# Performance work log

Hardware: AMD Instinct MI355X
Metric: run time of the kernel (lower is better)

The kernel has to match this reference:

```python
import jax, jax.numpy as jnp
import numpy as np
from jax import lax

T = 50
THETA = 1.0 - 0.0001  # max_1 - 0.0001, max_1 = T_win/T = 1.0


def conv_t(x, w, b, pad_h):
    # x: [N, C, H, W, T]; slayer conv3d has time-kernel 1 -> conv2d per timestep.
    n, c, h, wd, t = x.shape
    xb = jnp.moveaxis(x, -1, 1).reshape(n * t, c, h, wd)
    y = lax.conv_general_dilated(xb, w, (1, 1), [(pad_h, pad_h), (0, 0)])
    y = y + b[None, :, None, None]
    o, h2, w2 = y.shape[1], y.shape[2], y.shape[3]
    return jnp.moveaxis(y.reshape(n, t, o, h2, w2), 1, -1)


def if_spikes(a):
    # catCuda.getSpikes on an input stacked T times: IF neuron with constant
    # drive a per step, soft reset (v -= theta on spike). a: [N,C,H,W].
    def step(v, _):
        v = v + a
        s = (v >= THETA).astype(a.dtype)
        return v - s * THETA, s
    _, sp = lax.scan(step, jnp.zeros_like(a), None, length=T)
    return jnp.moveaxis(sp, 0, -1)  # [N,C,H,W,T]


def setup_inputs() -> dict:
    key = jax.random.key(0)
    ks = jax.random.split(key, 6)
    def w(k, shape, scale):
        return jax.random.normal(k, shape, jnp.float32) * scale
    x = jax.random.uniform(ks[0], (256, 1, 180, 1, T), jnp.float32)
    return {
        'x': x,
        'w1': w(ks[1], (16, 1, 3, 1), 0.3), 'b1': jnp.zeros(16, jnp.float32),
        'w2': w(ks[2], (32, 16, 9, 1), 0.1), 'b2': jnp.zeros(32, jnp.float32),
        'w3': w(ks[3], (32, 32, 7, 1), 0.1), 'b3': jnp.zeros(32, jnp.float32),
        'wf': w(ks[4], (4, 32, 83, 1), 0.05), 'bf': jnp.zeros(4, jnp.float32),
    }


def reference(x, w1, b1, w2, b2, w3, b3, wf, bf):
    y = conv_t(x, w1, b1, 1)                        # [N,16,180,1,T]
    y = if_spikes(jnp.sum(y, axis=4) / T)           # rate -> spikes
    y = conv_t(y, w2, b2, 1)                        # [N,32,174,1,T]
    y = if_spikes(jnp.sum(y, axis=4) / T)
    y = 1.1 * (y[:, :, 0::2] + y[:, :, 1::2])       # slayer sum-pool (2,1), weight 1.1
    y = if_spikes(jnp.sum(y, axis=4) / T)           # [N,32,87,1,T]
    y = conv_t(y, w3, b3, 1)                        # [N,32,83,1,T]
    y = if_spikes(jnp.sum(y, axis=4) / T)
    out = jnp.einsum('nchwt,ochw->not', y, wf) + bf[None, :, None]  # dense over full spatial
    return jnp.sum(out, axis=-1) / T                # sum_spikes / T -> [N,4]
```

## Files before the change

kernel.cpp:

```cpp
#include <hip/hip_runtime.h>


#define T_STEPS 50
#define THETA   0.9999f

__device__ __forceinline__ float spike_rate(float a, const float* __restrict__ tbl) {
    constexpr float INV = 50.0f / 0.9999f;
    float t = a * INV;
    float c = fminf(fmaxf(floorf(t), 0.0f), 50.0f);
    bool risky = (t > 0.5f) && (fabsf(t - rintf(t)) < 2e-4f);
    if (__ballot(risky)) {
        float v = 0.f, cnt = 0.f;
#pragma unroll 1
        for (int k = 0; k < T_STEPS; ++k) {
            v += a;
            float s = (v >= THETA) ? 1.0f : 0.0f;
            v -= s * THETA;
            cnt += s;
        }
        c = cnt;
    }
    return tbl[(int)c];
}

__device__ __forceinline__ float spike_rate_nb(float a, const float* __restrict__ tbl) {
    constexpr float INV = 50.0f / 0.9999f;
    float t = a * INV;
    float c = fminf(fmaxf(floorf(t), 0.0f), 50.0f);
    return tbl[(int)c];
}

extern "C" __global__ void __launch_bounds__(1024)
catnet_kernel(const float* __restrict__ x,
              const float* __restrict__ w1, const float* __restrict__ b1,
              const float* __restrict__ w2, const float* __restrict__ b2,
              const float* __restrict__ w3, const float* __restrict__ b3,
              const float* __restrict__ wf, const float* __restrict__ bf,
              float* __restrict__ out)
{
    const int n    = blockIdx.x;
    const int tid  = threadIdx.x;
    const int wave = tid >> 6;
    const int lane = tid & 63;

    __shared__ float xbar[182];
    __shared__ float r1pe[16][92];
    __shared__ float r1po[16][92];
    __shared__ float r3p[32][89];
    __shared__ alignas(16) float r4s[32][83];
    __shared__ float ratetbl[51];
    __shared__ float part[16];

    if (tid < 16)                { r1pe[tid][0] = 0.f; }
    if (tid >= 16 && tid < 32)   { r1po[tid-16][90] = 0.f; }
    if (tid >= 32 && tid < 64)   { r3p[tid-32][0] = 0.f; r3p[tid-32][88] = 0.f; }
    if (tid == 64)               { xbar[0] = 0.f; xbar[181] = 0.f; }
    if (tid >= 128 && tid < 179) { ratetbl[tid-128] = (float)(tid-128) / 50.0f; }

    const float* xn = x + (size_t)n * (180 * 50);
    if (tid < 720) {
        const int h = tid >> 2, q = tid & 3;
        const float2* row2 = reinterpret_cast<const float2*>(xn + h * 50);
        float s = 0.f;
        for (int k = q; k < 24; k += 4) { float2 v = row2[k]; s += v.x + v.y; }
        if (q == 0)                     { float2 v = row2[24]; s += v.x + v.y; }
        s += __shfl_xor(s, 1, 4);
        s += __shfl_xor(s, 2, 4);
        if (q == 0) xbar[h + 1] = s;
    }
    __syncthreads();

    for (int idx = tid; idx < 16 * 180; idx += 1024) {
        int c = idx / 180, h = idx - c * 180;
        float a = w1[c*3+0] * xbar[h] + w1[c*3+1] * xbar[h+1] + w1[c*3+2] * xbar[h+2];
        a = a / 50.0f + b1[c];
        float r = spike_rate(a, ratetbl);
        int H = h + 1;
        if (H & 1) r1po[c][H >> 1] = r;
        else       r1pe[c][H >> 1] = r;
    }
    __syncthreads();

    {
        const int g   = __builtin_amdgcn_readfirstlane(tid >> 7);
        const int p   = tid & 127;
        const bool act = p < 87;
        const int pr  = act ? p : 0;
        const float* wb = w2 + g * 4 * 144;

        float a0[4], a1[4];
#pragma unroll
        for (int j = 0; j < 4; ++j) { a0[j] = b2[g*4 + j]; a1[j] = a0[j]; }

        float we[5], wo[5];
#pragma unroll
        for (int d = 0; d < 5; ++d) { we[d] = r1pe[0][pr + d]; wo[d] = r1po[0][pr + d]; }

#pragma unroll 1
        for (int ci = 0; ci < 16; ++ci) {
            const int cn = (ci < 15) ? ci + 1 : 15;
            float weN[5], woN[5];
#pragma unroll
            for (int d = 0; d < 5; ++d) { weN[d] = r1pe[cn][pr + d]; woN[d] = r1po[cn][pr + d]; }

#pragma unroll
            for (int j = 0; j < 4; ++j) {
                const float* wj = wb + j * 144 + ci * 9;
#pragma unroll
                for (int kh = 0; kh < 9; ++kh) {
                    float wv  = wj[kh];
                    float xlo = (kh & 1) ? wo[kh >> 1] : we[kh >> 1];
                    float xhi = (kh & 1) ? we[(kh + 1) >> 1] : wo[kh >> 1];
                    a0[j] += wv * xlo;
                    a1[j] += wv * xhi;
                }
            }
#pragma unroll
            for (int d = 0; d < 5; ++d) { we[d] = weN[d]; wo[d] = woN[d]; }
        }
#pragma unroll
        for (int j = 0; j < 4; ++j) {
            float r20 = spike_rate(a0[j], ratetbl);
            float r21 = spike_rate(a1[j], ratetbl);
            float r3  = spike_rate_nb(1.1f * (r20 + r21), ratetbl);
            if (act) r3p[g*4 + j][p + 1] = r3;
        }
    }
    __syncthreads();

    {
        const int g4   = __builtin_amdgcn_readfirstlane((wave >> 1) * 4);
        const int half = wave & 1;
        const int cnt  = half ? 41 : 42;
        const bool act = lane < cnt;
        const int h0   = half * 42 + lane;
        const int hr   = act ? h0 : 0;
        const float* wb = w3 + g4 * 224;

        float a[4];
#pragma unroll
        for (int j = 0; j < 4; ++j) a[j] = b3[g4 + j];

        float rv[7];
#pragma unroll
        for (int kh = 0; kh < 7; ++kh) rv[kh] = r3p[0][hr + kh];

#pragma unroll 1
        for (int ci = 0; ci < 32; ++ci) {
            const int cn = (ci < 31) ? ci + 1 : 31;
            float rn[7];
#pragma unroll
            for (int kh = 0; kh < 7; ++kh) rn[kh] = r3p[cn][hr + kh];

#pragma unroll
            for (int j = 0; j < 4; ++j) {
                const float* wj = wb + j * 224 + ci * 7;
#pragma unroll
                for (int kh = 0; kh < 7; ++kh)
                    a[j] += wj[kh] * rv[kh];
            }
#pragma unroll
            for (int kh = 0; kh < 7; ++kh) rv[kh] = rn[kh];
        }
#pragma unroll
        for (int j = 0; j < 4; ++j) {
            float r = spike_rate(a[j], ratetbl);
            if (act) r4s[g4 + j][h0] = r;
        }
    }
    __syncthreads();

    {
        const int o = wave >> 2, q = wave & 3;
        const float2* r42 = reinterpret_cast<const float2*>(&r4s[0][0]);
        const float2* wo2 = reinterpret_cast<const float2*>(wf + o * (32 * 83));
        float acc = 0.f;
        for (int j = q * 64 + lane; j < 1328; j += 256) {
            float2 rv = r42[j], wv = wo2[j];
            acc += rv.x * wv.x + rv.y * wv.y;
        }
#pragma unroll
        for (int off = 32; off > 0; off >>= 1)
            acc += __shfl_down(acc, off, 64);
        if (lane == 0) part[wave] = acc;
    }
    __syncthreads();
    if (tid < 4) {
        float s = part[tid*4] + part[tid*4+1] + part[tid*4+2] + part[tid*4+3];
        out[n * 4 + tid] = s + bf[tid];
    }
}

extern "C" void kernel_launch(void* const* d_in, const int* in_sizes, int n_in,
                              void* d_out, int out_size, void* d_ws, size_t ws_size,
                              hipStream_t stream) {
    const float* x  = (const float*)d_in[0];
    const float* w1 = (const float*)d_in[1];
    const float* b1 = (const float*)d_in[2];
    const float* w2 = (const float*)d_in[3];
    const float* b2 = (const float*)d_in[4];
    const float* w3 = (const float*)d_in[5];
    const float* b3 = (const float*)d_in[6];
    const float* wf = (const float*)d_in[7];
    const float* bf = (const float*)d_in[8];
    float* outp = (float*)d_out;

    catnet_kernel<<<dim3(256), dim3(1024), 0, stream>>>(
        x, w1, b1, w2, b2, w3, b3, wf, bf, outp);
}
```

Measured before the change: 106.4 us.

## Split each sample across two blocks by spatial halves with halo recompute

Each batch sample is now handled by two 512-thread blocks, each computing one spatial half of the conv pipeline and recomputing the halo rows it needs from the earlier layers. Partial dense outputs go to a global buffer, and a second small kernel adds the two halves and the bias. This doubles the block count so the 256 compute units are better occupied and each block has less serial work. The cost is duplicated halo computation and an extra kernel launch with a global round trip.

```diff
diff --git a/kernel.cpp b/kernel.cpp
--- a/kernel.cpp
+++ b/kernel.cpp
@@ -3,6 +3,8 @@
 
 #define T_STEPS 50
 #define THETA   0.9999f
+
+__device__ float g_part[256 * 8];
 
 __device__ __forceinline__ float spike_rate(float a, const float* __restrict__ tbl) {
     constexpr float INV = 50.0f / 0.9999f;
@@ -30,18 +32,23 @@
     return tbl[(int)c];
 }
 
-extern "C" __global__ void __launch_bounds__(1024)
-catnet_kernel(const float* __restrict__ x,
-              const float* __restrict__ w1, const float* __restrict__ b1,
-              const float* __restrict__ w2, const float* __restrict__ b2,
-              const float* __restrict__ w3, const float* __restrict__ b3,
-              const float* __restrict__ wf, const float* __restrict__ bf,
-              float* __restrict__ out)
+extern "C" __global__ void __launch_bounds__(512, 4)
+catnet_split(const float* __restrict__ x,
+             const float* __restrict__ w1, const float* __restrict__ b1,
+             const float* __restrict__ w2, const float* __restrict__ b2,
+             const float* __restrict__ w3, const float* __restrict__ b3,
+             const float* __restrict__ wf)
 {
-    const int n    = blockIdx.x;
+    const int n    = blockIdx.x >> 1;
+    const int half = blockIdx.x & 1;
     const int tid  = threadIdx.x;
     const int wave = tid >> 6;
     const int lane = tid & 63;
+
+    const int x_lo   = half ? 80 : 0;   const int x_cnt  = half ? 100 : 104;
+    const int r1_lo  = half ? 81 : 0;   const int r1_cnt = half ?  99 : 103;
+    const int p_lo   = half ? 41 : 0;   const int p_cnt  = half ?  46 :  48;
+    const int h_lo   = half ? 42 : 0;   const int h_cnt  = half ?  41 :  42;
 
     __shared__ float xbar[182];
     __shared__ float r1pe[16][92];
@@ -49,7 +56,7 @@
     __shared__ float r3p[32][89];
     __shared__ alignas(16) float r4s[32][83];
     __shared__ float ratetbl[51];
-    __shared__ float part[16];
+    __shared__ float part[8];
 
     if (tid < 16)                { r1pe[tid][0] = 0.f; }
     if (tid >= 16 && tid < 32)   { r1po[tid-16][90] = 0.f; }
@@ -58,8 +65,9 @@
     if (tid >= 128 && tid < 179) { ratetbl[tid-128] = (float)(tid-128) / 50.0f; }
 
     const float* xn = x + (size_t)n * (180 * 50);
-    if (tid < 720) {
-        const int h = tid >> 2, q = tid & 3;
+    if (tid < 4 * x_cnt) {
+        const int h_l = tid >> 2, q = tid & 3;
+        const int h   = x_lo + h_l;
         const float2* row2 = reinterpret_cast<const float2*>(xn + h * 50);
         float s = 0.f;
         for (int k = q; k < 24; k += 4) { float2 v = row2[k]; s += v.x + v.y; }
@@ -70,22 +78,25 @@
     }
     __syncthreads();
 
-    for (int idx = tid; idx < 16 * 180; idx += 1024) {
-        int c = idx / 180, h = idx - c * 180;
+    for (int idx = tid; idx < 16 * 128; idx += 512) {
+        const int c = idx >> 7, h_l = idx & 127;
+        const bool act = h_l < r1_cnt;
+        const int h = r1_lo + (act ? h_l : 0);
         float a = w1[c*3+0] * xbar[h] + w1[c*3+1] * xbar[h+1] + w1[c*3+2] * xbar[h+2];
         a = a / 50.0f + b1[c];
         float r = spike_rate(a, ratetbl);
-        int H = h + 1;
-        if (H & 1) r1po[c][H >> 1] = r;
-        else       r1pe[c][H >> 1] = r;
+        if (act) {
+            int H = h + 1;
+            if (H & 1) r1po[c][H >> 1] = r;
+            else       r1pe[c][H >> 1] = r;
+        }
     }
     __syncthreads();
 
     {
-        const int g   = __builtin_amdgcn_readfirstlane(tid >> 7);
-        const int p   = tid & 127;
-        const bool act = p < 87;
-        const int pr  = act ? p : 0;
+        const int g   = __builtin_amdgcn_readfirstlane(wave);
+        const bool act = lane < p_cnt;
+        const int p   = p_lo + (act ? lane : 0);
         const float* wb = w2 + g * 4 * 144;
 
         float a0[4], a1[4];
@@ -94,14 +105,14 @@
 
         float we[5], wo[5];
 #pragma unroll
-        for (int d = 0; d < 5; ++d) { we[d] = r1pe[0][pr + d]; wo[d] = r1po[0][pr + d]; }
+        for (int d = 0; d < 5; ++d) { we[d] = r1pe[0][p + d]; wo[d] = r1po[0][p + d]; }
 
 #pragma unroll 1
         for (int ci = 0; ci < 16; ++ci) {
             const int cn = (ci < 15) ? ci + 1 : 15;
             float weN[5], woN[5];
 #pragma unroll
-            for (int d = 0; d < 5; ++d) { weN[d] = r1pe[cn][pr + d]; woN[d] = r1po[cn][pr + d]; }
+            for (int d = 0; d < 5; ++d) { weN[d] = r1pe[cn][p + d]; woN[d] = r1po[cn][p + d]; }
 
 #pragma unroll
             for (int j = 0; j < 4; ++j) {
@@ -129,12 +140,11 @@
     __syncthreads();
 
     {
-        const int g4   = __builtin_amdgcn_readfirstlane((wave >> 1) * 4);
-        const int half = wave & 1;
-        const int cnt  = half ? 41 : 42;
-        const bool act = lane < cnt;
-        const int h0   = half * 42 + lane;
-        const int hr   = act ? h0 : 0;
+        const int gg   = __builtin_amdgcn_readfirstlane(wave);
+        const int g4   = gg * 4;
+        const bool act = lane < h_cnt;
+        const int h0   = h_lo + lane;
+        const int hr   = act ? h0 : h_lo;
         const float* wb = w3 + g4 * 224;
 
         float a[4];
@@ -171,13 +181,13 @@
     __syncthreads();
 
     {
-        const int o = wave >> 2, q = wave & 3;
-        const float2* r42 = reinterpret_cast<const float2*>(&r4s[0][0]);
-        const float2* wo2 = reinterpret_cast<const float2*>(wf + o * (32 * 83));
+        const int o = wave >> 1, q = wave & 1;
         float acc = 0.f;
-        for (int j = q * 64 + lane; j < 1328; j += 256) {
-            float2 rv = r42[j], wv = wo2[j];
-            acc += rv.x * wv.x + rv.y * wv.y;
+        if (lane < h_cnt) {
+            const int h0 = h_lo + lane;
+            const float* wo = wf + o * (32 * 83);
+            for (int c = q; c < 32; c += 2)
+                acc += r4s[c][h0] * wo[c * 83 + h0];
         }
 #pragma unroll
         for (int off = 32; off > 0; off >>= 1)
@@ -185,9 +195,17 @@
         if (lane == 0) part[wave] = acc;
     }
     __syncthreads();
-    if (tid < 4) {
-        float s = part[tid*4] + part[tid*4+1] + part[tid*4+2] + part[tid*4+3];
-        out[n * 4 + tid] = s + bf[tid];
+    if (tid < 4)
+        g_part[n * 8 + half * 4 + tid] = part[2 * tid] + part[2 * tid + 1];
+}
+
+extern "C" __global__ void __launch_bounds__(256)
+catnet_finish(const float* __restrict__ bf, float* __restrict__ out)
+{
+    const int i = blockIdx.x * 256 + threadIdx.x;
+    if (i < 1024) {
+        const int n = i >> 2, o = i & 3;
+        out[i] = g_part[n * 8 + o] + g_part[n * 8 + 4 + o] + bf[o];
     }
 }
 
@@ -205,6 +223,7 @@
     const float* bf = (const float*)d_in[8];
     float* outp = (float*)d_out;
 
-    catnet_kernel<<<dim3(256), dim3(1024), 0, stream>>>(
-        x, w1, b1, w2, b2, w3, b3, wf, bf, outp);
-}
+    catnet_split<<<dim3(512), dim3(512), 0, stream>>>(
+        x, w1, b1, w2, b2, w3, b3, wf);
+    catnet_finish<<<dim3(4), dim3(256), 0, stream>>>(bf, outp);
+}
```

Result: no change. 107.4 us (+0.9%).

## Pack four channels per float4 in shared activations for vectorized LDS loads

Applied to the files above, without the earlier changes.

Rearranges the shared-memory activation buffers for conv2 and conv3 into channel-interleaved float4 arrays, so each thread fetches four input channels with one 128-bit LDS read. The loops now step over channel quads instead of single channels with prefetch. It also adds a min-blocks hint to launch_bounds. The aim is fewer LDS instructions and less load latency, in exchange for more live registers per quad and bank-conflict behaviour that may change.

```diff
diff --git a/kernel.cpp b/kernel.cpp
--- a/kernel.cpp
+++ b/kernel.cpp
@@ -3,6 +3,8 @@
 
 #define T_STEPS 50
 #define THETA   0.9999f
+
+#define F4C(v, c) ((c) == 0 ? (v).x : (c) == 1 ? (v).y : (c) == 2 ? (v).z : (v).w)
 
 __device__ __forceinline__ float spike_rate(float a, const float* __restrict__ tbl) {
     constexpr float INV = 50.0f / 0.9999f;
@@ -30,7 +32,7 @@
     return tbl[(int)c];
 }
 
-extern "C" __global__ void __launch_bounds__(1024)
+extern "C" __global__ void __launch_bounds__(1024, 4)
 catnet_kernel(const float* __restrict__ x,
               const float* __restrict__ w1, const float* __restrict__ b1,
               const float* __restrict__ w2, const float* __restrict__ b2,
@@ -43,19 +45,21 @@
     const int wave = tid >> 6;
     const int lane = tid & 63;
 
-    __shared__ float xbar[182];
-    __shared__ float r1pe[16][92];
-    __shared__ float r1po[16][92];
-    __shared__ float r3p[32][89];
+    __shared__ float  xbar[182];
+    __shared__ float4 r1qe[4][92];
+    __shared__ float4 r1qo[4][92];
+    __shared__ float4 r3q[8][89];
     __shared__ alignas(16) float r4s[32][83];
-    __shared__ float ratetbl[51];
-    __shared__ float part[16];
-
-    if (tid < 16)                { r1pe[tid][0] = 0.f; }
-    if (tid >= 16 && tid < 32)   { r1po[tid-16][90] = 0.f; }
-    if (tid >= 32 && tid < 64)   { r3p[tid-32][0] = 0.f; r3p[tid-32][88] = 0.f; }
-    if (tid == 64)               { xbar[0] = 0.f; xbar[181] = 0.f; }
-    if (tid >= 128 && tid < 179) { ratetbl[tid-128] = (float)(tid-128) / 50.0f; }
+    __shared__ float  ratetbl[51];
+    __shared__ float  part[16];
+
+    const float4 z4 = make_float4(0.f, 0.f, 0.f, 0.f);
+    if (tid < 4)               r1qe[tid][0]       = z4;
+    if (tid >= 4  && tid < 8)  r1qo[tid - 4][90]  = z4;
+    if (tid >= 8  && tid < 16) r3q[tid - 8][0]    = z4;
+    if (tid >= 16 && tid < 24) r3q[tid - 16][88]  = z4;
+    if (tid == 64)             { xbar[0] = 0.f; xbar[181] = 0.f; }
+    if (tid >= 128 && tid < 179) ratetbl[tid - 128] = (float)(tid - 128) / 50.0f;
 
     const float* xn = x + (size_t)n * (180 * 50);
     if (tid < 720) {
@@ -76,8 +80,9 @@
         a = a / 50.0f + b1[c];
         float r = spike_rate(a, ratetbl);
         int H = h + 1;
-        if (H & 1) r1po[c][H >> 1] = r;
-        else       r1pe[c][H >> 1] = r;
+        float* dst = (H & 1) ? (float*)&r1qo[c >> 2][H >> 1]
+                             : (float*)&r1qe[c >> 2][H >> 1];
+        dst[c & 3] = r;
     }
     __syncthreads();
 
@@ -92,44 +97,45 @@
 #pragma unroll
         for (int j = 0; j < 4; ++j) { a0[j] = b2[g*4 + j]; a1[j] = a0[j]; }
 
-        float we[5], wo[5];
-#pragma unroll
-        for (int d = 0; d < 5; ++d) { we[d] = r1pe[0][pr + d]; wo[d] = r1po[0][pr + d]; }
-
 #pragma unroll 1
-        for (int ci = 0; ci < 16; ++ci) {
-            const int cn = (ci < 15) ? ci + 1 : 15;
-            float weN[5], woN[5];
-#pragma unroll
-            for (int d = 0; d < 5; ++d) { weN[d] = r1pe[cn][pr + d]; woN[d] = r1po[cn][pr + d]; }
-
-#pragma unroll
-            for (int j = 0; j < 4; ++j) {
-                const float* wj = wb + j * 144 + ci * 9;
-#pragma unroll
-                for (int kh = 0; kh < 9; ++kh) {
-                    float wv  = wj[kh];
-                    float xlo = (kh & 1) ? wo[kh >> 1] : we[kh >> 1];
-                    float xhi = (kh & 1) ? we[(kh + 1) >> 1] : wo[kh >> 1];
-                    a0[j] += wv * xlo;
-                    a1[j] += wv * xhi;
+        for (int qd = 0; qd < 4; ++qd) {
+            float4 we[5], wo[5];
+#pragma unroll
+            for (int d = 0; d < 5; ++d) { we[d] = r1qe[qd][pr + d]; wo[d] = r1qo[qd][pr + d]; }
+
+#pragma unroll
+            for (int c4 = 0; c4 < 4; ++c4) {
+                const int ci = qd * 4 + c4;
+#pragma unroll
+                for (int j = 0; j < 4; ++j) {
+                    const float* wj = wb + j * 144 + ci * 9;
+#pragma unroll
+                    for (int kh = 0; kh < 9; ++kh) {
+                        float wv  = wj[kh];
+                        float xlo = (kh & 1) ? F4C(wo[kh >> 1], c4)
+                                             : F4C(we[kh >> 1], c4);
+                        float xhi = (kh & 1) ? F4C(we[(kh + 1) >> 1], c4)
+                                             : F4C(wo[kh >> 1], c4);
+                        a0[j] += wv * xlo;
+                        a1[j] += wv * xhi;
+                    }
                 }
             }
-#pragma unroll
-            for (int d = 0; d < 5; ++d) { we[d] = weN[d]; wo[d] = woN[d]; }
-        }
+        }
+        float r3t[4];
 #pragma unroll
         for (int j = 0; j < 4; ++j) {
             float r20 = spike_rate(a0[j], ratetbl);
             float r21 = spike_rate(a1[j], ratetbl);
-            float r3  = spike_rate_nb(1.1f * (r20 + r21), ratetbl);
-            if (act) r3p[g*4 + j][p + 1] = r3;
-        }
+            r3t[j] = spike_rate_nb(1.1f * (r20 + r21), ratetbl);
+        }
+        if (act) r3q[g][p + 1] = make_float4(r3t[0], r3t[1], r3t[2], r3t[3]);
     }
     __syncthreads();
 
     {
-        const int g4   = __builtin_amdgcn_readfirstlane((wave >> 1) * 4);
+        const int gg   = __builtin_amdgcn_readfirstlane(wave >> 1);
+        const int g4   = gg * 4;
         const int half = wave & 1;
         const int cnt  = half ? 41 : 42;
         const bool act = lane < cnt;
@@ -141,26 +147,23 @@
 #pragma unroll
         for (int j = 0; j < 4; ++j) a[j] = b3[g4 + j];
 
-        float rv[7];
-#pragma unroll
-        for (int kh = 0; kh < 7; ++kh) rv[kh] = r3p[0][hr + kh];
-
 #pragma unroll 1
-        for (int ci = 0; ci < 32; ++ci) {
-            const int cn = (ci < 31) ? ci + 1 : 31;
-            float rn[7];
-#pragma unroll
-            for (int kh = 0; kh < 7; ++kh) rn[kh] = r3p[cn][hr + kh];
-
-#pragma unroll
-            for (int j = 0; j < 4; ++j) {
-                const float* wj = wb + j * 224 + ci * 7;
-#pragma unroll
-                for (int kh = 0; kh < 7; ++kh)
-                    a[j] += wj[kh] * rv[kh];
+        for (int q = 0; q < 8; ++q) {
+            float4 rv[7];
+#pragma unroll
+            for (int d = 0; d < 7; ++d) rv[d] = r3q[q][hr + d];
+
+#pragma unroll
+            for (int c4 = 0; c4 < 4; ++c4) {
+                const int ci = q * 4 + c4;
+#pragma unroll
+                for (int j = 0; j < 4; ++j) {
+                    const float* wj = wb + j * 224 + ci * 7;
+#pragma unroll
+                    for (int kh = 0; kh < 7; ++kh)
+                        a[j] += wj[kh] * F4C(rv[kh], c4);
+                }
             }
-#pragma unroll
-            for (int kh = 0; kh < 7; ++kh) rv[kh] = rn[kh];
         }
 #pragma unroll
         for (int j = 0; j < 4; ++j) {
```

Result: faster. 99.15 us (-6.8%).
